# Kernel optimization log

Hardware: AMD Instinct MI355X
Metric: run time of the kernel (lower is better)

## Reference

```python
import jax, jax.numpy as jnp
import numpy as np

HIDDEN = 1024
NUM_HEADS = 16
HEAD_SIZE = HIDDEN // NUM_HEADS


def setup_inputs() -> dict:
    key = jax.random.key(0)
    ks = jax.random.split(key, 5)
    B, S = 2, 2048
    x = jax.random.normal(ks[0], (B, S, HIDDEN), dtype=jnp.float32)
    # nn.Linear(hidden, 3*hidden): weight stored (in, out) for x @ W
    scale_qkv = 1.0 / np.sqrt(HIDDEN)
    w_qkv = jax.random.uniform(ks[1], (HIDDEN, 3 * HIDDEN), minval=-scale_qkv, maxval=scale_qkv, dtype=jnp.float32)
    b_qkv = jax.random.uniform(ks[2], (3 * HIDDEN,), minval=-scale_qkv, maxval=scale_qkv, dtype=jnp.float32)
    w_o = jax.random.uniform(ks[3], (HIDDEN, HIDDEN), minval=-scale_qkv, maxval=scale_qkv, dtype=jnp.float32)
    b_o = jax.random.uniform(ks[4], (HIDDEN,), minval=-scale_qkv, maxval=scale_qkv, dtype=jnp.float32)
    return {"x": x, "w_qkv": w_qkv, "b_qkv": b_qkv, "w_o": w_o, "b_o": b_o}


def reference(x, w_qkv, b_qkv, w_o, b_o):
    B, S, H = x.shape
    qkv = x @ w_qkv + b_qkv  # (B, S, 3H)
    q, k, v = jnp.split(qkv, 3, axis=-1)
    # (B, S, H) -> (B, nheads, S, head_size)
    def heads(t):
        return t.reshape(B, S, NUM_HEADS, HEAD_SIZE).transpose(0, 2, 1, 3)
    q, k, v = heads(q), heads(k), heads(v)
    scores = jnp.einsum('bhqd,bhkd->bhqk', q, k) / np.sqrt(HEAD_SIZE).astype(np.float32)
    causal = jnp.tril(jnp.ones((S, S), dtype=bool))  # k <= q
    scores = jnp.where(causal, scores, -jnp.inf)
    probs = jax.nn.softmax(scores, axis=-1)
    out = jnp.einsum('bhqk,bhkd->bqhd', probs, v).reshape(B, S, H)
    return out @ w_o + b_o
```

## Files before the change

kernel.cpp:

```cpp
#include <hip/hip_runtime.h>
#include <stdint.h>


typedef __bf16 bf16;
typedef __attribute__((ext_vector_type(8))) __bf16 bf16x8;
typedef __attribute__((ext_vector_type(4))) __bf16 bf16x4;
typedef __attribute__((ext_vector_type(4))) float floatx4;
typedef __attribute__((ext_vector_type(16))) float floatx16;
typedef __attribute__((ext_vector_type(4))) unsigned int uint4v;
typedef __attribute__((ext_vector_type(2))) unsigned int uint2v;

#define SCL 0.18033688011112042f

__device__ __forceinline__ floatx4 mfma_bf16(bf16x8 a, bf16x8 b, floatx4 c) {
  return __builtin_amdgcn_mfma_f32_16x16x32_bf16(a, b, c, 0, 0, 0);
}

__device__ __forceinline__ floatx16 mfma32(bf16x8 a, bf16x8 b, floatx16 c) {
  return __builtin_amdgcn_mfma_f32_32x32x16_bf16(a, b, c, 0, 0, 0);
}

__device__ __forceinline__ void cp_g2l_16(const bf16* g, bf16* l) {
  __builtin_amdgcn_global_load_lds(
      (const __attribute__((address_space(1))) void*)g,
      (__attribute__((address_space(3))) void*)l, 16, 0, 0);
}

__device__ __forceinline__ floatx16 zero16() {
  floatx16 z;
#pragma unroll
  for (int i = 0; i < 16; ++i) z[i] = 0.f;
  return z;
}

__device__ __forceinline__ uint32_t pack2(float lo, float hi2) {
  union { bf16 h[2]; uint32_t u; } x;
  x.h[0] = (bf16)lo; x.h[1] = (bf16)hi2;
  return x.u;
}

__device__ __forceinline__ uint2v permswap(uint32_t a, uint32_t b) {
  return __builtin_amdgcn_permlane32_swap(a, b, false, false);
}

__device__ __forceinline__ bf16x8 mk_pf(uint32_t w0, uint32_t w1, uint32_t w2,
                                        uint32_t w3) {
  union { uint4v u; bf16x8 v; } c;
  c.u = (uint4v){w0, w1, w2, w3};
  return c.v;
}

__global__ __launch_bounds__(256) void prep_kernel(
    const float* __restrict__ x, bf16* __restrict__ xb,
    const float* __restrict__ w_qkv, bf16* __restrict__ wqkvt,
    const float* __restrict__ w_o, bf16* __restrict__ wot) {
  const int b = blockIdx.x;
  const int tid = threadIdx.x;
  if (b < 4096) {
    const int i = (b * 256 + tid) * 4;
    floatx4 v = *(const floatx4*)(x + i);
    bf16x4 o;
    o[0] = (bf16)v[0]; o[1] = (bf16)v[1]; o[2] = (bf16)v[2]; o[3] = (bf16)v[3];
    *(bf16x4*)(xb + i) = o;
    return;
  }
  __shared__ float tile[32][33];
  const float* W; bf16* Wt; int K, N, n0, k0;
  if (b < 7168) {
    const int bb = b - 4096;
    W = w_qkv; Wt = wqkvt; K = 1024; N = 3072;
    n0 = (bb % 96) * 32; k0 = (bb / 96) * 32;
  } else {
    const int bb = b - 7168;
    W = w_o; Wt = wot; K = 1024; N = 1024;
    n0 = (bb & 31) * 32; k0 = (bb >> 5) * 32;
  }
  const int tx = tid & 31, ty = tid >> 5;
  for (int i = 0; i < 4; ++i)
    tile[ty + 8 * i][tx] = W[(size_t)(k0 + ty + 8 * i) * N + n0 + tx];
  __syncthreads();
  for (int i = 0; i < 4; ++i)
    Wt[(size_t)(n0 + ty + 8 * i) * K + k0 + tx] = (bf16)tile[tx][ty + 8 * i];
}

template <int MODE, int MI>
__global__ __launch_bounds__(256, 3) void gemm_bt_kernel(
    const bf16* __restrict__ A, const bf16* __restrict__ Bt,
    const float* __restrict__ bias, float* __restrict__ outF,
    bf16* __restrict__ qb, bf16* __restrict__ kb, bf16* __restrict__ vtb,
    int N, int K) {
  constexpr int BM = MI * 32;
  __shared__ bf16 As[BM * 32];
  __shared__ bf16 Bs[128 * 32];
  const int tid = threadIdx.x;
  const int w = tid >> 6, lane = tid & 63;
  const int l16 = lane & 15, quad = lane >> 4;
  const int m0 = blockIdx.y * BM, n0 = blockIdx.x * 128;
  const int wm = (w & 1) * (BM / 2), wn = (w >> 1) * 64;

  const int arow = w * (BM / 4) + (lane >> 2);
  const int acol = (lane & 3) * 8;
  const bf16* Ag = A + (size_t)(m0 + arow) * K + acol;
  bf16* Al = As + arow * 32 + acol;
  const int brow = w * 32 + (lane >> 2);
  const bf16* Bg = Bt + (size_t)(n0 + brow) * K + acol;
  bf16* Bl = Bs + brow * 32 + acol;

  floatx4 acc[MI][4];
#pragma unroll
  for (int i = 0; i < MI; ++i)
#pragma unroll
    for (int j = 0; j < 4; ++j) acc[i][j] = (floatx4){0.f, 0.f, 0.f, 0.f};

  for (int k0 = 0; k0 < K; k0 += 32) {
    __syncthreads();
    cp_g2l_16(Ag + k0, Al);
    if (MI == 4) cp_g2l_16(Ag + (size_t)16 * K + k0, Al + 16 * 32);
    cp_g2l_16(Bg + k0, Bl);
    cp_g2l_16(Bg + (size_t)16 * K + k0, Bl + 16 * 32);
    __syncthreads();
    bf16x8 af[MI], bfr[4];
#pragma unroll
    for (int i = 0; i < MI; ++i)
      af[i] = *(const bf16x8*)(&As[(wm + i * 16 + l16) * 32 + quad * 8]);
#pragma unroll
    for (int j = 0; j < 4; ++j)
      bfr[j] = *(const bf16x8*)(&Bs[(wn + j * 16 + l16) * 32 + quad * 8]);
#pragma unroll
    for (int i = 0; i < MI; ++i)
#pragma unroll
      for (int j = 0; j < 4; ++j)
        acc[i][j] = mfma_bf16(af[i], bfr[j], acc[i][j]);
  }

#pragma unroll
  for (int i = 0; i < MI; ++i)
#pragma unroll
    for (int j = 0; j < 4; ++j) {
      const int nn = n0 + wn + j * 16 + l16;
      const float bv = bias[nn];
      const int mbase = m0 + wm + i * 16 + quad * 4;
      if (MODE == 1) {
#pragma unroll
        for (int r = 0; r < 4; ++r)
          outF[(size_t)(mbase + r) * N + nn] = acc[i][j][r] + bv;
      } else {
        const int which = nn >> 10;
        const int rem = nn & 1023;
        const int h = rem >> 6, d = rem & 63;
        const int b = mbase >> 11, s = mbase & 2047;
        const size_t bh = (size_t)(b * 16 + h);
        if (which == 2) {
          bf16x4 pk;
#pragma unroll
          for (int r = 0; r < 4; ++r) pk[r] = (bf16)(acc[i][j][r] + bv);
          *(bf16x4*)(vtb + (bh * 64 + d) * 2048 + s) = pk;
        } else if (which == 0) {
#pragma unroll
          for (int r = 0; r < 4; ++r)
            qb[(bh * 2048 + s + r) * 64 + d] = (bf16)((acc[i][j][r] + bv) * SCL);
        } else {
#pragma unroll
          for (int r = 0; r < 4; ++r)
            kb[(bh * 2048 + s + r) * 64 + d] = (bf16)(acc[i][j][r] + bv);
        }
      }
    }
}

__global__ __launch_bounds__(256, 4) void attn_kernel(
    const bf16* __restrict__ Qb, const bf16* __restrict__ Kb,
    const bf16* __restrict__ Vtb, bf16* __restrict__ attnb) {
  __shared__ bf16 Ks[3][4096];
  __shared__ bf16 Vs[2][4096];
  const int bid = blockIdx.x;
  const int c = bid & 255, qq = bid >> 8;
  const int bh = c & 31;
  const int kk = c >> 5;
  const int g = (qq == 0) ? kk : (qq == 1) ? 31 - kk
              : (qq == 2) ? 8 + kk : 23 - kk;
  const int tid = threadIdx.x;
  const int w = tid >> 6, lane = tid & 63;
  const int l31 = lane & 31, hi = lane >> 5;
  const int strip = w >> 1, ms = w & 1;
  const int q0s = g * 64 + strip * 32;
  const int b = bh >> 4, h = bh & 15;
  const int nt = g + 1;

  const bf16* Qh = Qb + (size_t)bh * 2048 * 64;
  const bf16* Kh = Kb + (size_t)bh * 2048 * 64;
  const bf16* Vh = Vtb + (size_t)bh * 64 * 2048;

  const int c0 = tid, c1 = tid + 256;
  const int kof0 = (c0 >> 3) * 64 + ((((c0 & 7) - (c0 >> 3)) & 7) * 8);
  const int kof1 = (c1 >> 3) * 64 + ((((c1 & 7) - (c1 >> 3)) & 7) * 8);
  const int vof0 = (c0 >> 3) * 2048 + ((((c0 & 7) - (c0 >> 3)) & 7) * 8);
  const int vof1 = (c1 >> 3) * 2048 + ((((c1 & 7) - (c1 >> 3)) & 7) * 8);

  bf16x8 qf[4];
  {
    const bf16* Qr = Qh + (size_t)(q0s + l31) * 64 + hi * 8;
#pragma unroll
    for (int kd = 0; kd < 4; ++kd) qf[kd] = *(const bf16x8*)(Qr + kd * 16);
  }
  bf16x8 ones;
#pragma unroll
  for (int j = 0; j < 8; ++j) ones[j] = (bf16)1.0f;

  floatx16 O0 = zero16(), O1 = zero16(), Ol = zero16();

  {
    const int k1 = (1 < nt) ? 1 : 0;
    cp_g2l_16(Kh + kof0, &Ks[0][c0 * 8]);
    cp_g2l_16(Kh + kof1, &Ks[0][c1 * 8]);
    cp_g2l_16(Kh + (size_t)k1 * 4096 + kof0, &Ks[1][c0 * 8]);
    cp_g2l_16(Kh + (size_t)k1 * 4096 + kof1, &Ks[1][c1 * 8]);
    cp_g2l_16(Vh + vof0, &Vs[0][c0 * 8]);
    cp_g2l_16(Vh + vof1, &Vs[0][c1 * 8]);
    asm volatile("s_waitcnt vmcnt(4)" ::: "memory");
    __builtin_amdgcn_sched_barrier(0);
  }

  int kr = 0;
  for (int t = 0; t < nt; ++t) {
    __builtin_amdgcn_s_barrier();
    __builtin_amdgcn_sched_barrier(0);

    {
      const int tk = (t + 2 < nt) ? t + 2 : 0;
      const int tv = (t + 1 < nt) ? t + 1 : 0;
      const int kst = (kr >= 1) ? kr - 1 : 2;
      cp_g2l_16(Kh + (size_t)tk * 4096 + kof0, &Ks[kst][c0 * 8]);
      cp_g2l_16(Kh + (size_t)tk * 4096 + kof1, &Ks[kst][c1 * 8]);
      cp_g2l_16(Vh + (size_t)tv * 64 + vof0, &Vs[(t + 1) & 1][c0 * 8]);
      cp_g2l_16(Vh + (size_t)tv * 64 + vof1, &Vs[(t + 1) & 1][c1 * 8]);
    }

    const bool diag = (t == g);
    if (!(diag && strip == 0 && ms == 1)) {
      const bf16* KsC = &Ks[kr][0];

      floatx16 sf = zero16();
      const int row = ms * 32 + l31;
      __builtin_amdgcn_s_setprio(1);
#pragma unroll
      for (int kd = 0; kd < 4; ++kd) {
        bf16x8 kf = *(const bf16x8*)(
            &KsC[row * 64 + (((kd * 2 + hi) + row) & 7) * 8]);
        sf = mfma32(kf, qf[kd], sf);
      }
      __builtin_amdgcn_s_setprio(0);

      float e[16];
#pragma unroll
      for (int r = 0; r < 16; ++r) {
        float s = sf[r];
        if (diag) {
          const int kc = t * 64 + ms * 32 + (r & 3) + 8 * (r >> 2) + 4 * hi;
          s = (kc <= q0s + l31) ? s : -1e30f;
        }
        e[r] = __builtin_amdgcn_exp2f(s);
      }

      uint32_t W[8];
#pragma unroll
      for (int i = 0; i < 8; ++i) W[i] = pack2(e[2 * i], e[2 * i + 1]);
      uint2v s0 = permswap(W[0], W[2]);
      uint2v s1 = permswap(W[1], W[3]);
      bf16x8 pa = mk_pf(s0.x, s1.x, s0.y, s1.y);
      uint2v s2 = permswap(W[4], W[6]);
      uint2v s3 = permswap(W[5], W[7]);
      bf16x8 pb = mk_pf(s2.x, s3.x, s2.y, s3.y);

      asm volatile("s_waitcnt vmcnt(4)" ::: "memory");
      __builtin_amdgcn_sched_barrier(0);

      const bf16* VsC = &Vs[t & 1][0];
      const int ksA = ms * 2, ksB = ms * 2 + 1;
      const int r0 = l31, r1 = 32 + l31;
      bf16x8 va0 = *(const bf16x8*)(&VsC[r0 * 64 + (((ksA * 2 + hi) + r0) & 7) * 8]);
      bf16x8 va1 = *(const bf16x8*)(&VsC[r1 * 64 + (((ksA * 2 + hi) + r1) & 7) * 8]);
      bf16x8 vb0 = *(const bf16x8*)(&VsC[r0 * 64 + (((ksB * 2 + hi) + r0) & 7) * 8]);
      bf16x8 vb1 = *(const bf16x8*)(&VsC[r1 * 64 + (((ksB * 2 + hi) + r1) & 7) * 8]);

      __builtin_amdgcn_s_setprio(1);
      O0 = mfma32(pa, va0, O0);
      O1 = mfma32(pa, va1, O1);
      Ol = mfma32(pa, ones, Ol);
      O0 = mfma32(pb, vb0, O0);
      O1 = mfma32(pb, vb1, O1);
      Ol = mfma32(pb, ones, Ol);
      __builtin_amdgcn_s_setprio(0);
    }
    kr = (kr == 2) ? 0 : kr + 1;
  }

  __syncthreads();
  float* fO = (float*)(&Ks[0][0]);
  float* fL = (float*)(&Vs[0][0]);
  if (ms == 1) {
#pragma unroll
    for (int r = 0; r < 16; ++r) {
      const int ql = (r & 3) + 8 * (r >> 2) + 4 * hi;
      fO[strip * 2048 + ql * 64 + l31] = O0[r];
      fO[strip * 2048 + ql * 64 + 32 + l31] = O1[r];
      if (l31 == 0) fL[strip * 32 + ql] = Ol[r];
    }
  }
  __syncthreads();
  if (ms == 0) {
#pragma unroll
    for (int r = 0; r < 16; ++r) {
      const int ql = (r & 3) + 8 * (r >> 2) + 4 * hi;
      const float o0 = O0[r] + fO[strip * 2048 + ql * 64 + l31];
      const float o1 = O1[r] + fO[strip * 2048 + ql * 64 + 32 + l31];
      const float inv = 1.f / (Ol[r] + fL[strip * 32 + ql]);
      bf16* dst = attnb + ((size_t)(b * 2048 + q0s + ql)) * 1024 + h * 64;
      dst[l31] = (bf16)(o0 * inv);
      dst[32 + l31] = (bf16)(o1 * inv);
    }
  }
}

extern "C" void kernel_launch(void* const* d_in, const int* in_sizes, int n_in,
                              void* d_out, int out_size, void* d_ws, size_t ws_size,
                              hipStream_t stream) {
  const float* x     = (const float*)d_in[0];
  const float* w_qkv = (const float*)d_in[1];
  const float* b_qkv = (const float*)d_in[2];
  const float* w_o   = (const float*)d_in[3];
  const float* b_o   = (const float*)d_in[4];
  float* out = (float*)d_out;

  char* ws = (char*)d_ws;
  bf16* xb    = (bf16*)ws; ws += (size_t)4096 * 1024 * 2;
  bf16* wqkvt = (bf16*)ws; ws += (size_t)3072 * 1024 * 2;
  bf16* wot   = (bf16*)ws; ws += (size_t)1024 * 1024 * 2;
  bf16* qb    = (bf16*)ws; ws += (size_t)32 * 2048 * 64 * 2;
  bf16* kb    = (bf16*)ws; ws += (size_t)32 * 2048 * 64 * 2;
  bf16* vtb   = (bf16*)ws; ws += (size_t)32 * 2048 * 64 * 2;
  bf16* attnb = (bf16*)ws; ws += (size_t)4096 * 1024 * 2;

  prep_kernel<<<8192, 256, 0, stream>>>(x, xb, w_qkv, wqkvt, w_o, wot);
  gemm_bt_kernel<0, 4><<<dim3(24, 32), 256, 0, stream>>>(
      xb, wqkvt, b_qkv, nullptr, qb, kb, vtb, 3072, 1024);
  attn_kernel<<<1024, 256, 0, stream>>>(qb, kb, vtb, attnb);
  gemm_bt_kernel<1, 2><<<dim3(8, 64), 256, 0, stream>>>(
      attnb, wot, b_o, out, nullptr, nullptr, nullptr, 1024, 1024);
}
```

Before: 170.9 us.

## Triple-buffer GEMM shared-memory tiles with async prefetch two stages ahead

The bf16 GEMM kernel now keeps three shared-memory buffers for the A and B tiles. It issues global-to-LDS loads two k-steps ahead and uses explicit vmcnt waits with a single barrier per step, replacing the two syncthreads per step. MFMA issue is wrapped in s_setprio to favour math waves. The goal is to hide global load latency behind compute, at the cost of tripling LDS use, which may lower occupancy with launch_bounds(256,3), and of issuing wasted dummy loads on the last steps.

Result: slower. 176.3 us (+3.2%).

```diff
diff --git a/kernel.cpp b/kernel.cpp
--- a/kernel.cpp
+++ b/kernel.cpp
@@ -90,8 +90,8 @@
     bf16* __restrict__ qb, bf16* __restrict__ kb, bf16* __restrict__ vtb,
     int N, int K) {
   constexpr int BM = MI * 32;
-  __shared__ bf16 As[BM * 32];
-  __shared__ bf16 Bs[128 * 32];
+  __shared__ bf16 As[3][BM * 32];
+  __shared__ bf16 Bs[3][128 * 32];
   const int tid = threadIdx.x;
   const int w = tid >> 6, lane = tid & 63;
   const int l16 = lane & 15, quad = lane >> 4;
@@ -101,10 +101,20 @@
   const int arow = w * (BM / 4) + (lane >> 2);
   const int acol = (lane & 3) * 8;
   const bf16* Ag = A + (size_t)(m0 + arow) * K + acol;
-  bf16* Al = As + arow * 32 + acol;
+  const int aoff = arow * 32 + acol;
   const int brow = w * 32 + (lane >> 2);
   const bf16* Bg = Bt + (size_t)(n0 + brow) * K + acol;
-  bf16* Bl = Bs + brow * 32 + acol;
+  const int boff = brow * 32 + acol;
+
+  const int nsteps = K / 32;
+
+  auto stage = [&](int kt, int bb) {
+    cp_g2l_16(Ag + kt * 32, &As[bb][aoff]);
+    if constexpr (MI == 4)
+      cp_g2l_16(Ag + (size_t)16 * K + kt * 32, &As[bb][aoff + 16 * 32]);
+    cp_g2l_16(Bg + kt * 32, &Bs[bb][boff]);
+    cp_g2l_16(Bg + (size_t)16 * K + kt * 32, &Bs[bb][boff + 16 * 32]);
+  };
 
   floatx4 acc[MI][4];
 #pragma unroll
@@ -112,26 +122,47 @@
 #pragma unroll
     for (int j = 0; j < 4; ++j) acc[i][j] = (floatx4){0.f, 0.f, 0.f, 0.f};
 
-  for (int k0 = 0; k0 < K; k0 += 32) {
-    __syncthreads();
-    cp_g2l_16(Ag + k0, Al);
-    if (MI == 4) cp_g2l_16(Ag + (size_t)16 * K + k0, Al + 16 * 32);
-    cp_g2l_16(Bg + k0, Bl);
-    cp_g2l_16(Bg + (size_t)16 * K + k0, Bl + 16 * 32);
-    __syncthreads();
+  stage(0, 0);
+  stage(1, 1);
+  if constexpr (MI == 4)
+    asm volatile("s_waitcnt vmcnt(4)" ::: "memory");
+  else
+    asm volatile("s_waitcnt vmcnt(3)" ::: "memory");
+  __builtin_amdgcn_sched_barrier(0);
+
+  int br = 0;
+  int bst = 2;
+  for (int t = 0; t < nsteps; ++t) {
+    __builtin_amdgcn_s_barrier();
+    __builtin_amdgcn_sched_barrier(0);
+
+    stage((t + 2 < nsteps) ? t + 2 : 0, bst);
+
     bf16x8 af[MI], bfr[4];
 #pragma unroll
     for (int i = 0; i < MI; ++i)
-      af[i] = *(const bf16x8*)(&As[(wm + i * 16 + l16) * 32 + quad * 8]);
+      af[i] = *(const bf16x8*)(&As[br][(wm + i * 16 + l16) * 32 + quad * 8]);
 #pragma unroll
     for (int j = 0; j < 4; ++j)
-      bfr[j] = *(const bf16x8*)(&Bs[(wn + j * 16 + l16) * 32 + quad * 8]);
+      bfr[j] = *(const bf16x8*)(&Bs[br][(wn + j * 16 + l16) * 32 + quad * 8]);
+    __builtin_amdgcn_s_setprio(1);
 #pragma unroll
     for (int i = 0; i < MI; ++i)
 #pragma unroll
       for (int j = 0; j < 4; ++j)
         acc[i][j] = mfma_bf16(af[i], bfr[j], acc[i][j]);
-  }
+    __builtin_amdgcn_s_setprio(0);
+
+    if constexpr (MI == 4)
+      asm volatile("s_waitcnt vmcnt(4)" ::: "memory");
+    else
+      asm volatile("s_waitcnt vmcnt(3)" ::: "memory");
+    __builtin_amdgcn_sched_barrier(0);
+
+    br = (br == 2) ? 0 : br + 1;
+    bst = (bst == 2) ? 0 : bst + 1;
+  }
+  asm volatile("s_waitcnt vmcnt(0)" ::: "memory");
 
 #pragma unroll
   for (int i = 0; i < MI; ++i)
```
